# Performance work log

Hardware: AMD Instinct MI355X
Metric: run time of the kernel (lower is better)

The kernel has to match this reference:

```python
import jax, jax.numpy as jnp
import numpy as np

S, B, M, N = 32, 2048, 16, 8
H = (M + N) * 10        # gru hidden = 240
IN = 2 * (M + N)        # dnn input = 48
O1 = 4 * M * N          # fc1 out = 512
TEMP = 0.1              # concrete-dropout temperature


def _cdrop(x, u, p_logit):
    # concrete (MC) dropout with learned rate p = sigmoid(p_logit), fixed noise u
    p = jax.nn.sigmoid(p_logit)
    z = jax.nn.sigmoid((p_logit + jnp.log(u) - jnp.log1p(-u)) / TEMP)
    return x * (1.0 - z) / (1.0 - p)


def _layer_reg(W, p_logit, fan_in):
    p = jax.nn.sigmoid(p_logit)
    w_reg = jnp.sum(W * W) / (1.0 - p)
    d_reg = fan_in * (p * jnp.log(p) + (1.0 - p) * jnp.log1p(-p))
    return w_reg + d_reg


def setup_inputs() -> dict:
    key = jax.random.key(0)
    ks = jax.random.split(key, 24)
    def rn(i, shape, s=1.0):
        return jax.random.normal(ks[i], shape, jnp.float32) * s
    def ru(i, shape):
        return jax.random.uniform(ks[i], shape, jnp.float32, minval=1e-4, maxval=1.0 - 1e-4)
    return dict(
        y_t=rn(0, (B, N)),
        x_ens=rn(1, (S, B, M), 0.1),
        x_prev_prev_mean=rn(2, (B, M), 0.1),
        x_pred_prev_mean=rn(3, (B, M), 0.1),
        y_prev=rn(4, (B, N)),
        h_ens=rn(5, (S, B, H)),
        F_mat=jnp.eye(M, dtype=jnp.float32) + rn(6, (M, M), 0.01),
        H_mat=rn(7, (N, M), 0.1),
        W_in=rn(8, (H, IN), 0.05), b_in=jnp.zeros((H,), jnp.float32),
        W_ih=rn(9, (3 * H, H), 0.05), b_ih=jnp.zeros((3 * H,), jnp.float32),
        W_hh=rn(10, (3 * H, H), 0.05), b_hh=jnp.zeros((3 * H,), jnp.float32),
        W_fc1=rn(11, (O1, H), 0.05), b_fc1=jnp.zeros((O1,), jnp.float32),
        W_fc2=rn(12, (M * N, O1), 0.05), b_fc2=jnp.zeros((M * N,), jnp.float32),
        p_in=jnp.float32(0.4055), p_fc1=jnp.float32(0.4055), p_fc2=jnp.float32(0.4055),
        u_in=ru(13, (S, B, IN)), u_fc1=ru(14, (S, B, H)), u_fc2=ru(15, (S, B, O1)),
    )


def reference(y_t, x_ens, x_prev_prev_mean, x_pred_prev_mean, y_prev, h_ens,
              F_mat, H_mat, W_in, b_in, W_ih, b_ih, W_hh, b_hh,
              W_fc1, b_fc1, W_fc2, b_fc2, p_in, p_fc1, p_fc2,
              u_in, u_fc1, u_fc2):
    # predict (linear dynamics f(x) = F x, observation h(x) = H x)
    x_pred_ens = jnp.einsum('sbm,km->sbk', x_ens, F_mat)          # [S,B,M]
    x_pred_mean = x_pred_ens.mean(axis=0)                          # [B,M]
    x_filt_prev_mean = x_ens.mean(axis=0)                          # [B,M]
    y_pred_mean = x_pred_mean @ H_mat.T                            # [B,N]
    innov = y_t - y_pred_mean
    feat = jnp.concatenate([x_filt_prev_mean - x_pred_prev_mean, innov,
                            x_filt_prev_mean - x_prev_prev_mean, y_t - y_prev], axis=-1)
    feat = jnp.broadcast_to(feat[None], (S, B, IN))                # shared across ensemble
    # DNN (vectorized over ensemble axis S instead of python loop)
    x1 = jax.nn.relu(_cdrop(feat, u_in, p_in) @ W_in.T + b_in)     # [S,B,H]
    gi = x1 @ W_ih.T + b_ih
    gh = h_ens @ W_hh.T + b_hh
    i_r, i_z, i_n = jnp.split(gi, 3, axis=-1)
    h_r, h_z, h_n = jnp.split(gh, 3, axis=-1)
    r = jax.nn.sigmoid(i_r + h_r)
    z = jax.nn.sigmoid(i_z + h_z)
    ng = jnp.tanh(i_n + r * h_n)
    h_new = (1.0 - z) * ng + z * h_ens                             # [S,B,H]
    x2 = jax.nn.relu(_cdrop(h_new, u_fc1, p_fc1) @ W_fc1.T + b_fc1)  # [S,B,O1]
    K_vec = _cdrop(x2, u_fc2, p_fc2) @ W_fc2.T + b_fc2             # [S,B,M*N]
    K = K_vec.reshape(S, B, M, N)
    x_filt = x_pred_ens + jnp.einsum('sbmn,bn->sbm', K, innov)
    reg_total = (_layer_reg(W_in, p_in, IN) + _layer_reg(W_fc1, p_fc1, H)
                 + _layer_reg(W_fc2, p_fc2, O1))
    raw_reg = jnp.broadcast_to(reg_total, (S,))
    return (x_filt, raw_reg)
```

## Files before the change

kernel.cpp:

```cpp
#include <hip/hip_runtime.h>

typedef __bf16 bf16x8 __attribute__((ext_vector_type(8)));
typedef float  f32x4  __attribute__((ext_vector_type(4)));

__device__ __forceinline__ f32x4 MFMA(bf16x8 a, bf16x8 b, f32x4 c) {
    return __builtin_amdgcn_mfma_f32_16x16x32_bf16(a, b, c, 0, 0, 0);
}

__device__ __forceinline__ unsigned short f2bfu(float f) {
    unsigned int u = __builtin_bit_cast(unsigned int, f);
    u += 0x7FFFu + ((u >> 16) & 1u);
    return (unsigned short)(u >> 16);
}
__device__ __forceinline__ float bf2f(unsigned short s) {
    unsigned int u = ((unsigned int)s) << 16;
    return __builtin_bit_cast(float, u);
}
__device__ __forceinline__ float sigm(float x) { return 1.f / (1.f + __expf(-x)); }
__device__ __forceinline__ float tanh_f(float x) { return 1.f - 2.f / (__expf(2.f * x) + 1.f); }
__device__ __forceinline__ float cdrop(float x, float u, float plog, float scale) {
    float t = (plog + __logf(u) - __logf(1.f - u)) * 10.f;
    float z = 1.f / (1.f + __expf(-t));
    return x * (1.f - z) * scale;
}

__global__ void k_zero(float* acc) {
    if (threadIdx.x < 4) acc[threadIdx.x] = 0.f;
}

__global__ void k_convert(const float* __restrict__ Win, const float* __restrict__ Wih,
                          const float* __restrict__ Whh, const float* __restrict__ Wfc1,
                          const float* __restrict__ Wfc2,
                          unsigned short* __restrict__ WinP, unsigned short* __restrict__ WihP,
                          unsigned short* __restrict__ WhhP, unsigned short* __restrict__ Wfc1P,
                          unsigned short* __restrict__ Wfc2b, float* __restrict__ acc) {
    __shared__ float s3[3];
    int tid = threadIdx.x;
    if (tid < 3) s3[tid] = 0.f;
    __syncthreads();
    int f = blockIdx.x * 256 + tid;
    float sq = 0.f; int mi = -1;
    if (f < 72576) {
        const float* src; unsigned short* dst;
        int row, wo, kreal, scols, didx;
        if (f < 1920) {
            int t = f >> 7, r = f & 127;
            int kk = r >> 6, qd = (r >> 4) & 3, ln = r & 15;
            row = t * 16 + ln; wo = kk * 32 + qd * 8;
            kreal = 48; scols = 48; src = Win; dst = WinP; didx = f * 8;
            if (wo < 48) mi = 0;
        } else if (f < 24960) {
            int i = f - 1920;
            int tp = i >> 9, r = i & 511;
            int kk = r >> 6, qd = (r >> 4) & 3, ln = r & 15;
            row = (tp / 15) * 240 + (tp % 15) * 16 + ln; wo = kk * 32 + qd * 8;
            kreal = 240; scols = 240; src = Wih; dst = WihP; didx = i * 8;
        } else if (f < 48000) {
            int i = f - 24960;
            int tp = i >> 9, r = i & 511;
            int kk = r >> 6, qd = (r >> 4) & 3, ln = r & 15;
            row = (tp / 15) * 240 + (tp % 15) * 16 + ln; wo = kk * 32 + qd * 8;
            kreal = 240; scols = 240; src = Whh; dst = WhhP; didx = i * 8;
        } else if (f < 64384) {
            int i = f - 48000;
            int t = i >> 9, r = i & 511;
            int kk = r >> 6, qd = (r >> 4) & 3, ln = r & 15;
            row = t * 16 + ln; wo = kk * 32 + qd * 8;
            kreal = 240; scols = 240; src = Wfc1; dst = Wfc1P; didx = i * 8;
            if (wo < 240) mi = 1;
        } else {
            int i = f - 64384;
            int t = i >> 10, r = i & 1023;
            int kk = r >> 6, qd = (r >> 4) & 3, ln = r & 15;
            row = t * 16 + ln; wo = kk * 32 + qd * 8;
            kreal = 512; scols = 512; src = Wfc2; dst = Wfc2b; didx = i * 8;
            mi = 2;
        }
        ushort4 o0 = {0, 0, 0, 0}, o1 = {0, 0, 0, 0};
        if (wo < kreal) {
            float4 v0 = *(const float4*)(src + (size_t)row * scols + wo);
            float4 v1 = *(const float4*)(src + (size_t)row * scols + wo + 4);
            o0.x = f2bfu(v0.x); o0.y = f2bfu(v0.y); o0.z = f2bfu(v0.z); o0.w = f2bfu(v0.w);
            o1.x = f2bfu(v1.x); o1.y = f2bfu(v1.y); o1.z = f2bfu(v1.z); o1.w = f2bfu(v1.w);
            sq = v0.x * v0.x + v0.y * v0.y + v0.z * v0.z + v0.w * v0.w
               + v1.x * v1.x + v1.y * v1.y + v1.z * v1.z + v1.w * v1.w;
        }
        *(ushort4*)(dst + didx) = o0;
        *(ushort4*)(dst + didx + 4) = o1;
    }
    if (mi >= 0) atomicAdd(&s3[mi], sq);
    __syncthreads();
    if (tid < 3) atomicAdd(&acc[tid], s3[tid]);
}

__global__ void k_colmean(const float* __restrict__ x_ens, float* __restrict__ xfpm) {
    int t = blockIdx.x * 256 + threadIdx.x;
    float s = 0.f;
    for (int ss = 0; ss < 32; ++ss) s += x_ens[ss * 32768 + t];
    xfpm[t] = s * (1.f / 32.f);
}

__global__ void k_feat(const float* __restrict__ xfpm, const float* __restrict__ F_mat,
                       const float* __restrict__ H_mat, const float* __restrict__ y_t,
                       const float* __restrict__ y_prev, const float* __restrict__ xppm,
                       const float* __restrict__ xpdm, float* __restrict__ feat,
                       float* __restrict__ innov) {
    int b = blockIdx.x * 256 + threadIdx.x;
    if (b >= 2048) return;
    float xm[16];
    #pragma unroll
    for (int m = 0; m < 16; ++m) xm[m] = xfpm[b * 16 + m];
    float xpm[16];
    #pragma unroll
    for (int k = 0; k < 16; ++k) {
        float a = 0.f;
        #pragma unroll
        for (int m = 0; m < 16; ++m) a += xm[m] * F_mat[k * 16 + m];
        xpm[k] = a;
    }
    #pragma unroll
    for (int n = 0; n < 8; ++n) {
        float a = 0.f;
        #pragma unroll
        for (int k = 0; k < 16; ++k) a += xpm[k] * H_mat[n * 16 + k];
        float inn = y_t[b * 8 + n] - a;
        innov[b * 8 + n] = inn;
        feat[b * 48 + 16 + n] = inn;
        feat[b * 48 + 40 + n] = y_t[b * 8 + n] - y_prev[b * 8 + n];
    }
    #pragma unroll
    for (int m = 0; m < 16; ++m) {
        feat[b * 48 + m]      = xm[m] - xpdm[b * 16 + m];
        feat[b * 48 + 24 + m] = xm[m] - xppm[b * 16 + m];
    }
}

__global__ __launch_bounds__(512, 2) void k_fused(
    const float* __restrict__ feat, const float* __restrict__ u_in_g,
    const float* __restrict__ h_ens, const float* __restrict__ u_fc1_g,
    const float* __restrict__ u_fc2_g,
    const unsigned short* __restrict__ WinP, const unsigned short* __restrict__ WihP,
    const unsigned short* __restrict__ WhhP, const unsigned short* __restrict__ Wfc1P,
    const unsigned short* __restrict__ Wfc2b,
    const float* __restrict__ b_in, const float* __restrict__ b_ih,
    const float* __restrict__ b_hh, const float* __restrict__ b_fc1,
    const float* __restrict__ b_fc2,
    const float* __restrict__ p_in_l, const float* __restrict__ p_fc1_l,
    const float* __restrict__ p_fc2_l,
    const float* __restrict__ innov_ws, const float* __restrict__ x_ens,
    const float* __restrict__ F_mat, float* __restrict__ out) {

    __shared__ __align__(16) char smem[59392];
    unsigned short* sAin = (unsigned short*)smem;
    unsigned short* sA1  = (unsigned short*)(smem + 4608);
    unsigned short* sA2  = (unsigned short*)(smem + 21504);
    unsigned short* sHd  = (unsigned short*)(smem + 38400);
    unsigned short* sA5  = (unsigned short*)smem;
    float* sInn = (float*)(smem + 55296);
    float* sF   = (float*)(smem + 56320);
    float* sOut = (float*)(smem + 57344);

    int tid = threadIdx.x;
    int lane = tid & 63, wave = tid >> 6;
    int blk = blockIdx.x;
    int r0 = blk * 32;
    int b0 = (blk & 63) * 32;
    float plog_in = p_in_l[0];  float sc_in = 1.f / (1.f - sigm(plog_in));
    float plog_f1 = p_fc1_l[0]; float sc_f1 = 1.f / (1.f - sigm(plog_f1));
    float plog_f2 = p_fc2_l[0]; float sc_f2 = 1.f / (1.f - sigm(plog_f2));

    if (tid < 384) {
        int row = tid / 12, k = (tid % 12) * 4;
        float4 f = *(const float4*)(feat + (b0 + row) * 48 + k);
        float4 u = *(const float4*)(u_in_g + (size_t)(r0 + row) * 48 + k);
        ushort4 o;
        o.x = f2bfu(cdrop(f.x, u.x, plog_in, sc_in));
        o.y = f2bfu(cdrop(f.y, u.y, plog_in, sc_in));
        o.z = f2bfu(cdrop(f.z, u.z, plog_in, sc_in));
        o.w = f2bfu(cdrop(f.w, u.w, plog_in, sc_in));
        *(ushort4*)(sAin + row * 72 + k) = o;
    }
    if (tid < 128) {
        int row = tid / 4, k = 48 + (tid % 4) * 4;
        ushort4 z4 = {0, 0, 0, 0};
        *(ushort4*)(sAin + row * 72 + k) = z4;
    }
    for (int c = tid; c < 1920; c += 512) {
        int row = c / 60, k = (c % 60) * 4;
        float4 h = *(const float4*)(h_ens + (size_t)(r0 + row) * 240 + k);
        ushort4 o;
        o.x = f2bfu(h.x); o.y = f2bfu(h.y); o.z = f2bfu(h.z); o.w = f2bfu(h.w);
        *(ushort4*)(sA2 + row * 264 + k) = o;
    }
    if (tid < 192) {
        int row = tid / 6, k = 240 + (tid % 6) * 4;
        ushort4 z4 = {0, 0, 0, 0};
        *(ushort4*)(sA2 + row * 264 + k) = z4;
        *(ushort4*)(sA1 + row * 264 + k) = z4;
        *(ushort4*)(sHd + row * 264 + k) = z4;
    }
    if (tid < 64) *(float4*)(sInn + tid * 4) = *(const float4*)(innov_ws + b0 * 8 + tid * 4);
    if (tid >= 64 && tid < 128) {
        int q = tid - 64;
        *(float4*)(sF + q * 4) = *(const float4*)(F_mat + q * 4);
    }
    __syncthreads();

    int ln = lane & 15, qd = lane >> 4;

    for (int t = wave; t < 15; t += 8) {
        int col = t * 16 + ln;
        float bias = b_in[col];
        f32x4 a0 = {0.f, 0.f, 0.f, 0.f}, a1v = {0.f, 0.f, 0.f, 0.f};
        #pragma unroll
        for (int kk = 0; kk < 2; ++kk) {
            bf16x8 b = *(const bf16x8*)(WinP + ((t * 2 + kk) * 64 + lane) * 8);
            bf16x8 x0 = *(const bf16x8*)(sAin + ln * 72 + kk * 32 + qd * 8);
            bf16x8 x1 = *(const bf16x8*)(sAin + (16 + ln) * 72 + kk * 32 + qd * 8);
            a0 = MFMA(x0, b, a0);
            a1v = MFMA(x1, b, a1v);
        }
        #pragma unroll
        for (int i = 0; i < 4; ++i) {
            int row = qd * 4 + i;
            float v0 = a0[i] + bias;
            float v1 = a1v[i] + bias;
            sA1[row * 264 + col]        = f2bfu(v0 > 0.f ? v0 : 0.f);
            sA1[(16 + row) * 264 + col] = f2bfu(v1 > 0.f ? v1 : 0.f);
        }
    }
    __syncthreads();

    for (int u = wave; u < 30; u += 8) {
        int t = u >> 1, sub = u & 1;
        int j = t * 16 + ln;
        float upf[4];
        #pragma unroll
        for (int i = 0; i < 4; ++i) {
            int row = sub * 16 + qd * 4 + i;
            upf[i] = u_fc1_g[(size_t)(r0 + row) * 240 + j];
        }
        float bir_b = b_ih[j], biz_b = b_ih[240 + j], bin_b = b_ih[480 + j];
        float bhr_b = b_hh[j], bhz_b = b_hh[240 + j], bhn_b = b_hh[480 + j];
        f32x4 air = {0,0,0,0}, aiz = {0,0,0,0}, ain = {0,0,0,0};
        f32x4 ahr = {0,0,0,0}, ahz = {0,0,0,0}, ahn = {0,0,0,0};
        #pragma unroll
        for (int kk = 0; kk < 8; ++kk) {
            int wb = ((t * 8 + kk) * 64 + lane) * 8;
            bf16x8 bir = *(const bf16x8*)(WihP + wb);
            bf16x8 biz = *(const bf16x8*)(WihP + 61440 + wb);
            bf16x8 bin_ = *(const bf16x8*)(WihP + 122880 + wb);
            bf16x8 bhr = *(const bf16x8*)(WhhP + wb);
            bf16x8 bhz = *(const bf16x8*)(WhhP + 61440 + wb);
            bf16x8 bhn = *(const bf16x8*)(WhhP + 122880 + wb);
            int ao = (sub * 16 + ln) * 264 + kk * 32 + qd * 8;
            bf16x8 a1f = *(const bf16x8*)(sA1 + ao);
            bf16x8 a2f = *(const bf16x8*)(sA2 + ao);
            air = MFMA(a1f, bir, air);
            aiz = MFMA(a1f, biz, aiz);
            ain = MFMA(a1f, bin_, ain);
            ahr = MFMA(a2f, bhr, ahr);
            ahz = MFMA(a2f, bhz, ahz);
            ahn = MFMA(a2f, bhn, ahn);
        }
        #pragma unroll
        for (int i = 0; i < 4; ++i) {
            int row = sub * 16 + qd * 4 + i;
            float rg = sigm(air[i] + bir_b + ahr[i] + bhr_b);
            float zg = sigm(aiz[i] + biz_b + ahz[i] + bhz_b);
            float ng = tanh_f(ain[i] + bin_b + rg * (ahn[i] + bhn_b));
            float hp = bf2f(sA2[row * 264 + j]);
            float hn2 = (1.f - zg) * ng + zg * hp;
            sHd[row * 264 + j] = f2bfu(cdrop(hn2, upf[i], plog_f1, sc_f1));
        }
    }
    __syncthreads();

    for (int t = wave; t < 32; t += 8) {
        int col = t * 16 + ln;
        float u0[4], u1[4];
        #pragma unroll
        for (int i = 0; i < 4; ++i) {
            u0[i] = u_fc2_g[(size_t)(r0 + qd * 4 + i) * 512 + col];
            u1[i] = u_fc2_g[(size_t)(r0 + 16 + qd * 4 + i) * 512 + col];
        }
        float bias = b_fc1[col];
        f32x4 a0 = {0.f, 0.f, 0.f, 0.f}, a1v = {0.f, 0.f, 0.f, 0.f};
        #pragma unroll
        for (int kk = 0; kk < 8; ++kk) {
            bf16x8 b = *(const bf16x8*)(Wfc1P + ((t * 8 + kk) * 64 + lane) * 8);
            int ao = ln * 264 + kk * 32 + qd * 8;
            bf16x8 x0 = *(const bf16x8*)(sHd + ao);
            bf16x8 x1 = *(const bf16x8*)(sHd + 16 * 264 + ao);
            a0 = MFMA(x0, b, a0);
            a1v = MFMA(x1, b, a1v);
        }
        #pragma unroll
        for (int i = 0; i < 4; ++i) {
            int row = qd * 4 + i;
            float v0 = a0[i] + bias; v0 = v0 > 0.f ? v0 : 0.f;
            float v1 = a1v[i] + bias; v1 = v1 > 0.f ? v1 : 0.f;
            sA5[row * 520 + col]        = f2bfu(cdrop(v0, u0[i], plog_f2, sc_f2));
            sA5[(16 + row) * 520 + col] = f2bfu(cdrop(v1, u1[i], plog_f2, sc_f2));
        }
    }
    __syncthreads();

    {
        int t = wave;
        int j = t * 16 + ln;
        float bias = b_fc2[j];
        int n = lane & 7;
        int m = 2 * t + ((lane >> 3) & 1);
        f32x4 a0 = {0.f, 0.f, 0.f, 0.f}, a1v = {0.f, 0.f, 0.f, 0.f};
        #pragma unroll
        for (int kk = 0; kk < 16; ++kk) {
            bf16x8 b = *(const bf16x8*)(Wfc2b + ((t * 16 + kk) * 64 + lane) * 8);
            int ao = ln * 520 + kk * 32 + qd * 8;
            bf16x8 x0 = *(const bf16x8*)(sA5 + ao);
            bf16x8 x1 = *(const bf16x8*)(sA5 + 16 * 520 + ao);
            a0 = MFMA(x0, b, a0);
            a1v = MFMA(x1, b, a1v);
        }
        auto epi2 = [&](int sub, f32x4 accv) {
            #pragma unroll
            for (int i = 0; i < 4; ++i) {
                int row = sub * 16 + qd * 4 + i;
                float kv = accv[i] + bias;
                float pr = kv * sInn[row * 8 + n];
                pr += __shfl_xor(pr, 1);
                pr += __shfl_xor(pr, 2);
                pr += __shfl_xor(pr, 4);
                if (n == 0) sOut[row * 16 + m] = pr;
            }
        };
        epi2(0, a0);
        epi2(1, a1v);
    }
    __syncthreads();

    if (tid < 32) {
        int row = tid;
        float x[16];
        #pragma unroll
        for (int q = 0; q < 4; ++q)
            *(float4*)(x + q * 4) = *(const float4*)(x_ens + (size_t)(r0 + row) * 16 + q * 4);
        #pragma unroll
        for (int mq = 0; mq < 4; ++mq) {
            float4 o;
            float* op = (float*)&o;
            #pragma unroll
            for (int mm = 0; mm < 4; ++mm) {
                int m = mq * 4 + mm;
                float a = 0.f;
                #pragma unroll
                for (int k2 = 0; k2 < 16; ++k2) a += sF[m * 16 + k2] * x[k2];
                op[mm] = a + sOut[row * 16 + m];
            }
            *(float4*)(out + (size_t)(r0 + row) * 16 + mq * 4) = o;
        }
    }
}

__global__ void k_reg(const float* __restrict__ acc, const float* __restrict__ pin,
                      const float* __restrict__ pfc1, const float* __restrict__ pfc2,
                      float* __restrict__ out) {
    float fan[3] = {48.f, 240.f, 512.f};
    float pl[3] = {pin[0], pfc1[0], pfc2[0]};
    float reg = 0.f;
    for (int i = 0; i < 3; ++i) {
        float p = 1.f / (1.f + expf(-pl[i]));
        reg += acc[i] / (1.f - p) + fan[i] * (p * logf(p) + (1.f - p) * logf(1.f - p));
    }
    if (threadIdx.x < 32) out[1048576 + threadIdx.x] = reg;
}

extern "C" void kernel_launch(void* const* d_in, const int* in_sizes, int n_in,
                              void* d_out, int out_size, void* d_ws, size_t ws_size,
                              hipStream_t stream) {
    const float* y_t    = (const float*)d_in[0];
    const float* x_ens  = (const float*)d_in[1];
    const float* xppm   = (const float*)d_in[2];
    const float* xpdm   = (const float*)d_in[3];
    const float* y_prev = (const float*)d_in[4];
    const float* h_ens  = (const float*)d_in[5];
    const float* F_mat  = (const float*)d_in[6];
    const float* H_mat  = (const float*)d_in[7];
    const float* W_in   = (const float*)d_in[8];
    const float* b_in   = (const float*)d_in[9];
    const float* W_ih   = (const float*)d_in[10];
    const float* b_ih   = (const float*)d_in[11];
    const float* W_hh   = (const float*)d_in[12];
    const float* b_hh   = (const float*)d_in[13];
    const float* W_fc1  = (const float*)d_in[14];
    const float* b_fc1  = (const float*)d_in[15];
    const float* W_fc2  = (const float*)d_in[16];
    const float* b_fc2  = (const float*)d_in[17];
    const float* p_in   = (const float*)d_in[18];
    const float* p_fc1  = (const float*)d_in[19];
    const float* p_fc2  = (const float*)d_in[20];
    const float* u_in   = (const float*)d_in[21];
    const float* u_fc1  = (const float*)d_in[22];
    const float* u_fc2  = (const float*)d_in[23];

    char* ws = (char*)d_ws;
    float* acc            = (float*)(ws + 0);
    unsigned short* WinP  = (unsigned short*)(ws + 64);
    unsigned short* WihP  = (unsigned short*)(ws + 30784);
    unsigned short* WhhP  = (unsigned short*)(ws + 399424);
    unsigned short* Wfc1P = (unsigned short*)(ws + 768064);
    unsigned short* Wfc2b = (unsigned short*)(ws + 1030208);
    float* xfpm           = (float*)(ws + 1161280);
    float* feat           = (float*)(ws + 1292352);
    float* innov          = (float*)(ws + 1685568);
    float* out = (float*)d_out;

    k_zero<<<1, 64, 0, stream>>>(acc);
    k_convert<<<284, 256, 0, stream>>>(W_in, W_ih, W_hh, W_fc1, W_fc2,
                                       WinP, WihP, WhhP, Wfc1P, Wfc2b, acc);
    k_colmean<<<128, 256, 0, stream>>>(x_ens, xfpm);
    k_feat<<<8, 256, 0, stream>>>(xfpm, F_mat, H_mat, y_t, y_prev, xppm, xpdm, feat, innov);
    k_fused<<<2048, 512, 0, stream>>>(feat, u_in, h_ens, u_fc1, u_fc2,
                                      WinP, WihP, WhhP, Wfc1P, Wfc2b,
                                      b_in, b_ih, b_hh, b_fc1, b_fc2,
                                      p_in, p_fc1, p_fc2, innov, x_ens, F_mat, out);
    k_reg<<<1, 64, 0, stream>>>(acc, p_in, p_fc1, p_fc2, out);
}
```

Baseline: 491.0 us.

## Halve row tile per block to 16 rows with 256 threads and more blocks

The fused kernel now processes 16 ensemble-batch rows per block with 4 waves instead of 32 rows with 8 waves, launching twice as many blocks. Shared memory roughly halves and the launch bounds now allow more resident blocks per CU. This aims at higher occupancy and better latency hiding. The cost is that each weight fragment loaded from global/L2 feeds only one MFMA row tile instead of two, which doubles total weight traffic.

```diff
diff --git a/kernel.cpp b/kernel.cpp
--- a/kernel.cpp
+++ b/kernel.cpp
@@ -135,7 +135,7 @@
     }
 }
 
-__global__ __launch_bounds__(512, 2) void k_fused(
+__global__ __launch_bounds__(256, 5) void k_fused(
     const float* __restrict__ feat, const float* __restrict__ u_in_g,
     const float* __restrict__ h_ens, const float* __restrict__ u_fc1_g,
     const float* __restrict__ u_fc2_g,
@@ -150,26 +150,26 @@
     const float* __restrict__ innov_ws, const float* __restrict__ x_ens,
     const float* __restrict__ F_mat, float* __restrict__ out) {
 
-    __shared__ __align__(16) char smem[59392];
+    __shared__ __align__(16) char smem[30208];
     unsigned short* sAin = (unsigned short*)smem;
-    unsigned short* sA1  = (unsigned short*)(smem + 4608);
-    unsigned short* sA2  = (unsigned short*)(smem + 21504);
-    unsigned short* sHd  = (unsigned short*)(smem + 38400);
+    unsigned short* sA1  = (unsigned short*)(smem + 2304);
+    unsigned short* sA2  = (unsigned short*)(smem + 10752);
+    unsigned short* sHd  = (unsigned short*)(smem + 19200);
     unsigned short* sA5  = (unsigned short*)smem;
-    float* sInn = (float*)(smem + 55296);
-    float* sF   = (float*)(smem + 56320);
-    float* sOut = (float*)(smem + 57344);
+    float* sInn = (float*)(smem + 27648);
+    float* sF   = (float*)(smem + 28160);
+    float* sOut = (float*)(smem + 29184);
 
     int tid = threadIdx.x;
     int lane = tid & 63, wave = tid >> 6;
     int blk = blockIdx.x;
-    int r0 = blk * 32;
-    int b0 = (blk & 63) * 32;
+    int r0 = blk * 16;
+    int b0 = (blk & 127) * 16;
     float plog_in = p_in_l[0];  float sc_in = 1.f / (1.f - sigm(plog_in));
     float plog_f1 = p_fc1_l[0]; float sc_f1 = 1.f / (1.f - sigm(plog_f1));
     float plog_f2 = p_fc2_l[0]; float sc_f2 = 1.f / (1.f - sigm(plog_f2));
 
-    if (tid < 384) {
+    if (tid < 192) {
         int row = tid / 12, k = (tid % 12) * 4;
         float4 f = *(const float4*)(feat + (b0 + row) * 48 + k);
         float4 u = *(const float4*)(u_in_g + (size_t)(r0 + row) * 48 + k);
@@ -180,64 +180,59 @@
         o.w = f2bfu(cdrop(f.w, u.w, plog_in, sc_in));
         *(ushort4*)(sAin + row * 72 + k) = o;
     }
-    if (tid < 128) {
+    if (tid < 64) {
         int row = tid / 4, k = 48 + (tid % 4) * 4;
         ushort4 z4 = {0, 0, 0, 0};
         *(ushort4*)(sAin + row * 72 + k) = z4;
     }
-    for (int c = tid; c < 1920; c += 512) {
+    for (int c = tid; c < 960; c += 256) {
         int row = c / 60, k = (c % 60) * 4;
         float4 h = *(const float4*)(h_ens + (size_t)(r0 + row) * 240 + k);
         ushort4 o;
         o.x = f2bfu(h.x); o.y = f2bfu(h.y); o.z = f2bfu(h.z); o.w = f2bfu(h.w);
         *(ushort4*)(sA2 + row * 264 + k) = o;
     }
-    if (tid < 192) {
+    if (tid < 96) {
         int row = tid / 6, k = 240 + (tid % 6) * 4;
         ushort4 z4 = {0, 0, 0, 0};
         *(ushort4*)(sA2 + row * 264 + k) = z4;
         *(ushort4*)(sA1 + row * 264 + k) = z4;
         *(ushort4*)(sHd + row * 264 + k) = z4;
     }
-    if (tid < 64) *(float4*)(sInn + tid * 4) = *(const float4*)(innov_ws + b0 * 8 + tid * 4);
-    if (tid >= 64 && tid < 128) {
-        int q = tid - 64;
+    if (tid < 32) *(float4*)(sInn + tid * 4) = *(const float4*)(innov_ws + b0 * 8 + tid * 4);
+    if (tid >= 32 && tid < 96) {
+        int q = tid - 32;
         *(float4*)(sF + q * 4) = *(const float4*)(F_mat + q * 4);
     }
     __syncthreads();
 
     int ln = lane & 15, qd = lane >> 4;
 
-    for (int t = wave; t < 15; t += 8) {
+    for (int t = wave; t < 15; t += 4) {
         int col = t * 16 + ln;
         float bias = b_in[col];
-        f32x4 a0 = {0.f, 0.f, 0.f, 0.f}, a1v = {0.f, 0.f, 0.f, 0.f};
+        f32x4 a0 = {0.f, 0.f, 0.f, 0.f};
         #pragma unroll
         for (int kk = 0; kk < 2; ++kk) {
             bf16x8 b = *(const bf16x8*)(WinP + ((t * 2 + kk) * 64 + lane) * 8);
             bf16x8 x0 = *(const bf16x8*)(sAin + ln * 72 + kk * 32 + qd * 8);
-            bf16x8 x1 = *(const bf16x8*)(sAin + (16 + ln) * 72 + kk * 32 + qd * 8);
             a0 = MFMA(x0, b, a0);
-            a1v = MFMA(x1, b, a1v);
         }
         #pragma unroll
         for (int i = 0; i < 4; ++i) {
             int row = qd * 4 + i;
             float v0 = a0[i] + bias;
-            float v1 = a1v[i] + bias;
-            sA1[row * 264 + col]        = f2bfu(v0 > 0.f ? v0 : 0.f);
-            sA1[(16 + row) * 264 + col] = f2bfu(v1 > 0.f ? v1 : 0.f);
-        }
-    }
-    __syncthreads();
-
-    for (int u = wave; u < 30; u += 8) {
-        int t = u >> 1, sub = u & 1;
+            sA1[row * 264 + col] = f2bfu(v0 > 0.f ? v0 : 0.f);
+        }
+    }
+    __syncthreads();
+
+    for (int t = wave; t < 15; t += 4) {
         int j = t * 16 + ln;
         float upf[4];
         #pragma unroll
         for (int i = 0; i < 4; ++i) {
-            int row = sub * 16 + qd * 4 + i;
+            int row = qd * 4 + i;
             upf[i] = u_fc1_g[(size_t)(r0 + row) * 240 + j];
         }
         float bir_b = b_ih[j], biz_b = b_ih[240 + j], bin_b = b_ih[480 + j];
@@ -253,7 +248,7 @@
             bf16x8 bhr = *(const bf16x8*)(WhhP + wb);
             bf16x8 bhz = *(const bf16x8*)(WhhP + 61440 + wb);
             bf16x8 bhn = *(const bf16x8*)(WhhP + 122880 + wb);
-            int ao = (sub * 16 + ln) * 264 + kk * 32 + qd * 8;
+            int ao = ln * 264 + kk * 32 + qd * 8;
             bf16x8 a1f = *(const bf16x8*)(sA1 + ao);
             bf16x8 a2f = *(const bf16x8*)(sA2 + ao);
             air = MFMA(a1f, bir, air);
@@ -265,7 +260,7 @@
         }
         #pragma unroll
         for (int i = 0; i < 4; ++i) {
-            int row = sub * 16 + qd * 4 + i;
+            int row = qd * 4 + i;
             float rg = sigm(air[i] + bir_b + ahr[i] + bhr_b);
             float zg = sigm(aiz[i] + biz_b + ahz[i] + bhz_b);
             float ng = tanh_f(ain[i] + bin_b + rg * (ahn[i] + bhn_b));
@@ -276,70 +271,55 @@
     }
     __syncthreads();
 
-    for (int t = wave; t < 32; t += 8) {
+    for (int t = wave; t < 32; t += 4) {
         int col = t * 16 + ln;
-        float u0[4], u1[4];
-        #pragma unroll
-        for (int i = 0; i < 4; ++i) {
+        float u0[4];
+        #pragma unroll
+        for (int i = 0; i < 4; ++i)
             u0[i] = u_fc2_g[(size_t)(r0 + qd * 4 + i) * 512 + col];
-            u1[i] = u_fc2_g[(size_t)(r0 + 16 + qd * 4 + i) * 512 + col];
-        }
         float bias = b_fc1[col];
-        f32x4 a0 = {0.f, 0.f, 0.f, 0.f}, a1v = {0.f, 0.f, 0.f, 0.f};
+        f32x4 a0 = {0.f, 0.f, 0.f, 0.f};
         #pragma unroll
         for (int kk = 0; kk < 8; ++kk) {
             bf16x8 b = *(const bf16x8*)(Wfc1P + ((t * 8 + kk) * 64 + lane) * 8);
-            int ao = ln * 264 + kk * 32 + qd * 8;
-            bf16x8 x0 = *(const bf16x8*)(sHd + ao);
-            bf16x8 x1 = *(const bf16x8*)(sHd + 16 * 264 + ao);
+            bf16x8 x0 = *(const bf16x8*)(sHd + ln * 264 + kk * 32 + qd * 8);
             a0 = MFMA(x0, b, a0);
-            a1v = MFMA(x1, b, a1v);
         }
         #pragma unroll
         for (int i = 0; i < 4; ++i) {
             int row = qd * 4 + i;
             float v0 = a0[i] + bias; v0 = v0 > 0.f ? v0 : 0.f;
-            float v1 = a1v[i] + bias; v1 = v1 > 0.f ? v1 : 0.f;
-            sA5[row * 520 + col]        = f2bfu(cdrop(v0, u0[i], plog_f2, sc_f2));
-            sA5[(16 + row) * 520 + col] = f2bfu(cdrop(v1, u1[i], plog_f2, sc_f2));
-        }
-    }
-    __syncthreads();
-
-    {
-        int t = wave;
+            sA5[row * 520 + col] = f2bfu(cdrop(v0, u0[i], plog_f2, sc_f2));
+        }
+    }
+    __syncthreads();
+
+    for (int t = wave; t < 8; t += 4) {
         int j = t * 16 + ln;
         float bias = b_fc2[j];
         int n = lane & 7;
         int m = 2 * t + ((lane >> 3) & 1);
-        f32x4 a0 = {0.f, 0.f, 0.f, 0.f}, a1v = {0.f, 0.f, 0.f, 0.f};
+        f32x4 a0 = {0.f, 0.f, 0.f, 0.f};
         #pragma unroll
         for (int kk = 0; kk < 16; ++kk) {
             bf16x8 b = *(const bf16x8*)(Wfc2b + ((t * 16 + kk) * 64 + lane) * 8);
-            int ao = ln * 520 + kk * 32 + qd * 8;
-            bf16x8 x0 = *(const bf16x8*)(sA5 + ao);
-            bf16x8 x1 = *(const bf16x8*)(sA5 + 16 * 520 + ao);
+            bf16x8 x0 = *(const bf16x8*)(sA5 + ln * 520 + kk * 32 + qd * 8);
             a0 = MFMA(x0, b, a0);
-            a1v = MFMA(x1, b, a1v);
-        }
-        auto epi2 = [&](int sub, f32x4 accv) {
-            #pragma unroll
-            for (int i = 0; i < 4; ++i) {
-                int row = sub * 16 + qd * 4 + i;
-                float kv = accv[i] + bias;
-                float pr = kv * sInn[row * 8 + n];
-                pr += __shfl_xor(pr, 1);
-                pr += __shfl_xor(pr, 2);
-                pr += __shfl_xor(pr, 4);
-                if (n == 0) sOut[row * 16 + m] = pr;
-            }
-        };
-        epi2(0, a0);
-        epi2(1, a1v);
-    }
-    __syncthreads();
-
-    if (tid < 32) {
+        }
+        #pragma unroll
+        for (int i = 0; i < 4; ++i) {
+            int row = qd * 4 + i;
+            float kv = a0[i] + bias;
+            float pr = kv * sInn[row * 8 + n];
+            pr += __shfl_xor(pr, 1);
+            pr += __shfl_xor(pr, 2);
+            pr += __shfl_xor(pr, 4);
+            if (n == 0) sOut[row * 16 + m] = pr;
+        }
+    }
+    __syncthreads();
+
+    if (tid < 16) {
         int row = tid;
         float x[16];
         #pragma unroll
@@ -420,7 +400,7 @@
                                        WinP, WihP, WhhP, Wfc1P, Wfc2b, acc);
     k_colmean<<<128, 256, 0, stream>>>(x_ens, xfpm);
     k_feat<<<8, 256, 0, stream>>>(xfpm, F_mat, H_mat, y_t, y_prev, xppm, xpdm, feat, innov);
-    k_fused<<<2048, 512, 0, stream>>>(feat, u_in, h_ens, u_fc1, u_fc2,
+    k_fused<<<4096, 256, 0, stream>>>(feat, u_in, h_ens, u_fc1, u_fc2,
                                       WinP, WihP, WhhP, Wfc1P, Wfc2b,
                                       b_in, b_ih, b_hh, b_fc1, b_fc2,
                                       p_in, p_fc1, p_fc2, innov, x_ens, F_mat, out);
```

After: 623.0 us. 1.27x slower.

## Merge setup kernels and fold regularizer reduction into fused kernel

Applied to the files above, without the earlier changes.

Weight conversion, ensemble column mean and feature computation now run in a single setup kernel, with block ranges split by role. The zero, colmean, feat and reg launches are removed. Global atomics are replaced by per-block partial sums that the first block of the main kernel reduces to produce the regularizer output. This cuts launch count and serialization gaps, at the cost of slightly more work in one block of the main kernel.

```diff
diff --git a/kernel.cpp b/kernel.cpp
--- a/kernel.cpp
+++ b/kernel.cpp
@@ -24,114 +24,118 @@
     return x * (1.f - z) * scale;
 }
 
-__global__ void k_zero(float* acc) {
-    if (threadIdx.x < 4) acc[threadIdx.x] = 0.f;
-}
-
-__global__ void k_convert(const float* __restrict__ Win, const float* __restrict__ Wih,
-                          const float* __restrict__ Whh, const float* __restrict__ Wfc1,
-                          const float* __restrict__ Wfc2,
-                          unsigned short* __restrict__ WinP, unsigned short* __restrict__ WihP,
-                          unsigned short* __restrict__ WhhP, unsigned short* __restrict__ Wfc1P,
-                          unsigned short* __restrict__ Wfc2b, float* __restrict__ acc) {
+__global__ void k_setup(const float* __restrict__ Win, const float* __restrict__ Wih,
+                        const float* __restrict__ Whh, const float* __restrict__ Wfc1,
+                        const float* __restrict__ Wfc2,
+                        unsigned short* __restrict__ WinP, unsigned short* __restrict__ WihP,
+                        unsigned short* __restrict__ WhhP, unsigned short* __restrict__ Wfc1P,
+                        unsigned short* __restrict__ Wfc2b, float* __restrict__ part,
+                        const float* __restrict__ x_ens, const float* __restrict__ F_mat,
+                        const float* __restrict__ H_mat, const float* __restrict__ y_t,
+                        const float* __restrict__ y_prev, const float* __restrict__ xppm,
+                        const float* __restrict__ xpdm, float* __restrict__ feat,
+                        float* __restrict__ innov) {
     __shared__ float s3[3];
     int tid = threadIdx.x;
-    if (tid < 3) s3[tid] = 0.f;
-    __syncthreads();
-    int f = blockIdx.x * 256 + tid;
-    float sq = 0.f; int mi = -1;
-    if (f < 72576) {
-        const float* src; unsigned short* dst;
-        int row, wo, kreal, scols, didx;
-        if (f < 1920) {
-            int t = f >> 7, r = f & 127;
-            int kk = r >> 6, qd = (r >> 4) & 3, ln = r & 15;
-            row = t * 16 + ln; wo = kk * 32 + qd * 8;
-            kreal = 48; scols = 48; src = Win; dst = WinP; didx = f * 8;
-            if (wo < 48) mi = 0;
-        } else if (f < 24960) {
-            int i = f - 1920;
-            int tp = i >> 9, r = i & 511;
-            int kk = r >> 6, qd = (r >> 4) & 3, ln = r & 15;
-            row = (tp / 15) * 240 + (tp % 15) * 16 + ln; wo = kk * 32 + qd * 8;
-            kreal = 240; scols = 240; src = Wih; dst = WihP; didx = i * 8;
-        } else if (f < 48000) {
-            int i = f - 24960;
-            int tp = i >> 9, r = i & 511;
-            int kk = r >> 6, qd = (r >> 4) & 3, ln = r & 15;
-            row = (tp / 15) * 240 + (tp % 15) * 16 + ln; wo = kk * 32 + qd * 8;
-            kreal = 240; scols = 240; src = Whh; dst = WhhP; didx = i * 8;
-        } else if (f < 64384) {
-            int i = f - 48000;
-            int t = i >> 9, r = i & 511;
-            int kk = r >> 6, qd = (r >> 4) & 3, ln = r & 15;
-            row = t * 16 + ln; wo = kk * 32 + qd * 8;
-            kreal = 240; scols = 240; src = Wfc1; dst = Wfc1P; didx = i * 8;
-            if (wo < 240) mi = 1;
-        } else {
-            int i = f - 64384;
-            int t = i >> 10, r = i & 1023;
-            int kk = r >> 6, qd = (r >> 4) & 3, ln = r & 15;
-            row = t * 16 + ln; wo = kk * 32 + qd * 8;
-            kreal = 512; scols = 512; src = Wfc2; dst = Wfc2b; didx = i * 8;
-            mi = 2;
-        }
-        ushort4 o0 = {0, 0, 0, 0}, o1 = {0, 0, 0, 0};
-        if (wo < kreal) {
-            float4 v0 = *(const float4*)(src + (size_t)row * scols + wo);
-            float4 v1 = *(const float4*)(src + (size_t)row * scols + wo + 4);
-            o0.x = f2bfu(v0.x); o0.y = f2bfu(v0.y); o0.z = f2bfu(v0.z); o0.w = f2bfu(v0.w);
-            o1.x = f2bfu(v1.x); o1.y = f2bfu(v1.y); o1.z = f2bfu(v1.z); o1.w = f2bfu(v1.w);
-            sq = v0.x * v0.x + v0.y * v0.y + v0.z * v0.z + v0.w * v0.w
-               + v1.x * v1.x + v1.y * v1.y + v1.z * v1.z + v1.w * v1.w;
-        }
-        *(ushort4*)(dst + didx) = o0;
-        *(ushort4*)(dst + didx + 4) = o1;
-    }
-    if (mi >= 0) atomicAdd(&s3[mi], sq);
-    __syncthreads();
-    if (tid < 3) atomicAdd(&acc[tid], s3[tid]);
-}
-
-__global__ void k_colmean(const float* __restrict__ x_ens, float* __restrict__ xfpm) {
-    int t = blockIdx.x * 256 + threadIdx.x;
-    float s = 0.f;
-    for (int ss = 0; ss < 32; ++ss) s += x_ens[ss * 32768 + t];
-    xfpm[t] = s * (1.f / 32.f);
-}
-
-__global__ void k_feat(const float* __restrict__ xfpm, const float* __restrict__ F_mat,
-                       const float* __restrict__ H_mat, const float* __restrict__ y_t,
-                       const float* __restrict__ y_prev, const float* __restrict__ xppm,
-                       const float* __restrict__ xpdm, float* __restrict__ feat,
-                       float* __restrict__ innov) {
-    int b = blockIdx.x * 256 + threadIdx.x;
-    if (b >= 2048) return;
-    float xm[16];
-    #pragma unroll
-    for (int m = 0; m < 16; ++m) xm[m] = xfpm[b * 16 + m];
-    float xpm[16];
-    #pragma unroll
-    for (int k = 0; k < 16; ++k) {
-        float a = 0.f;
-        #pragma unroll
-        for (int m = 0; m < 16; ++m) a += xm[m] * F_mat[k * 16 + m];
-        xpm[k] = a;
-    }
-    #pragma unroll
-    for (int n = 0; n < 8; ++n) {
-        float a = 0.f;
-        #pragma unroll
-        for (int k = 0; k < 16; ++k) a += xpm[k] * H_mat[n * 16 + k];
-        float inn = y_t[b * 8 + n] - a;
-        innov[b * 8 + n] = inn;
-        feat[b * 48 + 16 + n] = inn;
-        feat[b * 48 + 40 + n] = y_t[b * 8 + n] - y_prev[b * 8 + n];
-    }
-    #pragma unroll
-    for (int m = 0; m < 16; ++m) {
-        feat[b * 48 + m]      = xm[m] - xpdm[b * 16 + m];
-        feat[b * 48 + 24 + m] = xm[m] - xppm[b * 16 + m];
+    int blk = blockIdx.x;
+    if (blk < 284) {
+        if (tid < 3) s3[tid] = 0.f;
+        __syncthreads();
+        int f = blk * 256 + tid;
+        float sq = 0.f; int mi = -1;
+        if (f < 72576) {
+            const float* src; unsigned short* dst;
+            int row, wo, kreal, scols, didx;
+            if (f < 1920) {
+                int t = f >> 7, r = f & 127;
+                int kk = r >> 6, qd = (r >> 4) & 3, ln = r & 15;
+                row = t * 16 + ln; wo = kk * 32 + qd * 8;
+                kreal = 48; scols = 48; src = Win; dst = WinP; didx = f * 8;
+                if (wo < 48) mi = 0;
+            } else if (f < 24960) {
+                int i = f - 1920;
+                int tp = i >> 9, r = i & 511;
+                int kk = r >> 6, qd = (r >> 4) & 3, ln = r & 15;
+                row = (tp / 15) * 240 + (tp % 15) * 16 + ln; wo = kk * 32 + qd * 8;
+                kreal = 240; scols = 240; src = Wih; dst = WihP; didx = i * 8;
+            } else if (f < 48000) {
+                int i = f - 24960;
+                int tp = i >> 9, r = i & 511;
+                int kk = r >> 6, qd = (r >> 4) & 3, ln = r & 15;
+                row = (tp / 15) * 240 + (tp % 15) * 16 + ln; wo = kk * 32 + qd * 8;
+                kreal = 240; scols = 240; src = Whh; dst = WhhP; didx = i * 8;
+            } else if (f < 64384) {
+                int i = f - 48000;
+                int t = i >> 9, r = i & 511;
+                int kk = r >> 6, qd = (r >> 4) & 3, ln = r & 15;
+                row = t * 16 + ln; wo = kk * 32 + qd * 8;
+                kreal = 240; scols = 240; src = Wfc1; dst = Wfc1P; didx = i * 8;
+                if (wo < 240) mi = 1;
+            } else {
+                int i = f - 64384;
+                int t = i >> 10, r = i & 1023;
+                int kk = r >> 6, qd = (r >> 4) & 3, ln = r & 15;
+                row = t * 16 + ln; wo = kk * 32 + qd * 8;
+                kreal = 512; scols = 512; src = Wfc2; dst = Wfc2b; didx = i * 8;
+                mi = 2;
+            }
+            ushort4 o0 = {0, 0, 0, 0}, o1 = {0, 0, 0, 0};
+            if (wo < kreal) {
+                float4 v0 = *(const float4*)(src + (size_t)row * scols + wo);
+                float4 v1 = *(const float4*)(src + (size_t)row * scols + wo + 4);
+                o0.x = f2bfu(v0.x); o0.y = f2bfu(v0.y); o0.z = f2bfu(v0.z); o0.w = f2bfu(v0.w);
+                o1.x = f2bfu(v1.x); o1.y = f2bfu(v1.y); o1.z = f2bfu(v1.z); o1.w = f2bfu(v1.w);
+                sq = v0.x * v0.x + v0.y * v0.y + v0.z * v0.z + v0.w * v0.w
+                   + v1.x * v1.x + v1.y * v1.y + v1.z * v1.z + v1.w * v1.w;
+            }
+            *(ushort4*)(dst + didx) = o0;
+            *(ushort4*)(dst + didx + 4) = o1;
+        }
+        if (mi >= 0) atomicAdd(&s3[mi], sq);
+        __syncthreads();
+        if (tid < 3) part[tid * 284 + blk] = s3[tid];
+    } else {
+        int b = (blk - 284) * 256 + tid;
+        float4 a0 = {0.f, 0.f, 0.f, 0.f}, a1 = a0, a2 = a0, a3 = a0;
+        for (int ss = 0; ss < 32; ++ss) {
+            const float* p = x_ens + (size_t)ss * 32768 + b * 16;
+            float4 v0 = *(const float4*)(p + 0);
+            float4 v1 = *(const float4*)(p + 4);
+            float4 v2 = *(const float4*)(p + 8);
+            float4 v3 = *(const float4*)(p + 12);
+            a0.x += v0.x; a0.y += v0.y; a0.z += v0.z; a0.w += v0.w;
+            a1.x += v1.x; a1.y += v1.y; a1.z += v1.z; a1.w += v1.w;
+            a2.x += v2.x; a2.y += v2.y; a2.z += v2.z; a2.w += v2.w;
+            a3.x += v3.x; a3.y += v3.y; a3.z += v3.z; a3.w += v3.w;
+        }
+        float xm[16];
+        *(float4*)(xm + 0)  = a0; *(float4*)(xm + 4)  = a1;
+        *(float4*)(xm + 8)  = a2; *(float4*)(xm + 12) = a3;
+        #pragma unroll
+        for (int m = 0; m < 16; ++m) xm[m] *= (1.f / 32.f);
+        float xpm[16];
+        #pragma unroll
+        for (int k = 0; k < 16; ++k) {
+            float a = 0.f;
+            #pragma unroll
+            for (int m = 0; m < 16; ++m) a += xm[m] * F_mat[k * 16 + m];
+            xpm[k] = a;
+        }
+        #pragma unroll
+        for (int n = 0; n < 8; ++n) {
+            float a = 0.f;
+            #pragma unroll
+            for (int k = 0; k < 16; ++k) a += xpm[k] * H_mat[n * 16 + k];
+            float inn = y_t[b * 8 + n] - a;
+            innov[b * 8 + n] = inn;
+            feat[b * 48 + 16 + n] = inn;
+            feat[b * 48 + 40 + n] = y_t[b * 8 + n] - y_prev[b * 8 + n];
+        }
+        #pragma unroll
+        for (int m = 0; m < 16; ++m) {
+            feat[b * 48 + m]      = xm[m] - xpdm[b * 16 + m];
+            feat[b * 48 + 24 + m] = xm[m] - xppm[b * 16 + m];
+        }
     }
 }
 
@@ -148,7 +152,8 @@
     const float* __restrict__ p_in_l, const float* __restrict__ p_fc1_l,
     const float* __restrict__ p_fc2_l,
     const float* __restrict__ innov_ws, const float* __restrict__ x_ens,
-    const float* __restrict__ F_mat, float* __restrict__ out) {
+    const float* __restrict__ F_mat, const float* __restrict__ part,
+    float* __restrict__ out) {
 
     __shared__ __align__(16) char smem[59392];
     unsigned short* sAin = (unsigned short*)smem;
@@ -168,6 +173,27 @@
     float plog_in = p_in_l[0];  float sc_in = 1.f / (1.f - sigm(plog_in));
     float plog_f1 = p_fc1_l[0]; float sc_f1 = 1.f / (1.f - sigm(plog_f1));
     float plog_f2 = p_fc2_l[0]; float sc_f2 = 1.f / (1.f - sigm(plog_f2));
+
+    if (blk == 0 && wave == 0) {
+        float s[3];
+        #pragma unroll
+        for (int i = 0; i < 3; ++i) {
+            float a = 0.f;
+            for (int l = lane; l < 284; l += 64) a += part[i * 284 + l];
+            #pragma unroll
+            for (int off = 32; off; off >>= 1) a += __shfl_xor(a, off);
+            s[i] = a;
+        }
+        float fan[3] = {48.f, 240.f, 512.f};
+        float pl[3] = {plog_in, plog_f1, plog_f2};
+        float reg = 0.f;
+        #pragma unroll
+        for (int i = 0; i < 3; ++i) {
+            float p = 1.f / (1.f + __expf(-pl[i]));
+            reg += s[i] / (1.f - p) + fan[i] * (p * __logf(p) + (1.f - p) * __logf(1.f - p));
+        }
+        if (lane < 32) out[1048576 + lane] = reg;
+    }
 
     if (tid < 384) {
         int row = tid / 12, k = (tid % 12) * 4;
@@ -360,19 +386,6 @@
             *(float4*)(out + (size_t)(r0 + row) * 16 + mq * 4) = o;
         }
     }
-}
-
-__global__ void k_reg(const float* __restrict__ acc, const float* __restrict__ pin,
-                      const float* __restrict__ pfc1, const float* __restrict__ pfc2,
-                      float* __restrict__ out) {
-    float fan[3] = {48.f, 240.f, 512.f};
-    float pl[3] = {pin[0], pfc1[0], pfc2[0]};
-    float reg = 0.f;
-    for (int i = 0; i < 3; ++i) {
-        float p = 1.f / (1.f + expf(-pl[i]));
-        reg += acc[i] / (1.f - p) + fan[i] * (p * logf(p) + (1.f - p) * logf(1.f - p));
-    }
-    if (threadIdx.x < 32) out[1048576 + threadIdx.x] = reg;
 }
 
 extern "C" void kernel_launch(void* const* d_in, const int* in_sizes, int n_in,
@@ -404,25 +417,22 @@
     const float* u_fc2  = (const float*)d_in[23];
 
     char* ws = (char*)d_ws;
-    float* acc            = (float*)(ws + 0);
     unsigned short* WinP  = (unsigned short*)(ws + 64);
     unsigned short* WihP  = (unsigned short*)(ws + 30784);
     unsigned short* WhhP  = (unsigned short*)(ws + 399424);
     unsigned short* Wfc1P = (unsigned short*)(ws + 768064);
     unsigned short* Wfc2b = (unsigned short*)(ws + 1030208);
-    float* xfpm           = (float*)(ws + 1161280);
     float* feat           = (float*)(ws + 1292352);
     float* innov          = (float*)(ws + 1685568);
+    float* part           = (float*)(ws + 1751104);
     float* out = (float*)d_out;
 
-    k_zero<<<1, 64, 0, stream>>>(acc);
-    k_convert<<<284, 256, 0, stream>>>(W_in, W_ih, W_hh, W_fc1, W_fc2,
-                                       WinP, WihP, WhhP, Wfc1P, Wfc2b, acc);
-    k_colmean<<<128, 256, 0, stream>>>(x_ens, xfpm);
-    k_feat<<<8, 256, 0, stream>>>(xfpm, F_mat, H_mat, y_t, y_prev, xppm, xpdm, feat, innov);
+    k_setup<<<292, 256, 0, stream>>>(W_in, W_ih, W_hh, W_fc1, W_fc2,
+                                     WinP, WihP, WhhP, Wfc1P, Wfc2b, part,
+                                     x_ens, F_mat, H_mat, y_t, y_prev, xppm, xpdm,
+                                     feat, innov);
     k_fused<<<2048, 512, 0, stream>>>(feat, u_in, h_ens, u_fc1, u_fc2,
                                       WinP, WihP, WhhP, Wfc1P, Wfc2b,
                                       b_in, b_ih, b_hh, b_fc1, b_fc2,
-                                      p_in, p_fc1, p_fc2, innov, x_ens, F_mat, out);
-    k_reg<<<1, 64, 0, stream>>>(acc, p_in, p_fc1, p_fc2, out);
-}
+                                      p_in, p_fc1, p_fc2, innov, x_ens, F_mat, part, out);
+}
```

Result: no change. 492.9 us (+0.4%).
